# Kernel optimization log

Hardware: AMD Instinct MI355X
Metric: run time of the kernel (lower is better)

The kernel has to match this reference:

```python
import jax, jax.numpy as jnp
import numpy as np

N_NODES = 100000
N_EDGES = 1600000
IN_CH = 128
OUT_CH = 64

def setup_inputs() -> dict:
    key = jax.random.key(0)
    k = jax.random.split(key, 7)
    x = jax.random.normal(k[0], (N_NODES, IN_CH), dtype=jnp.float32)
    edge_index = jax.random.randint(k[1], (2, N_EDGES), 0, N_NODES, dtype=jnp.int64)
    neg_edge_index = jax.random.randint(k[2], (2, N_EDGES), 0, N_NODES, dtype=jnp.int64)
    # GCNConv weight [in, out] + bias, Linear classifier [2*out, 2] + bias
    W = jax.random.normal(k[3], (IN_CH, OUT_CH), dtype=jnp.float32) / np.sqrt(IN_CH)
    b = jnp.zeros((OUT_CH,), dtype=jnp.float32)
    Wc = jax.random.normal(k[4], (2 * OUT_CH, 2), dtype=jnp.float32) / np.sqrt(2 * OUT_CH)
    bc = jnp.zeros((2,), dtype=jnp.float32)
    return {"x": x, "edge_index": edge_index, "neg_edge_index": neg_edge_index,
            "W": W, "b": b, "Wc": Wc, "bc": bc}

def reference(x, edge_index, neg_edge_index, W, b, Wc, bc):
    N = x.shape[0]
    # --- GCNConv: linear transform, add self-loops, symmetric deg normalization ---
    h = x @ W                                   # [N, out]
    loops = jnp.arange(N, dtype=edge_index.dtype)
    row = jnp.concatenate([edge_index[0], loops])   # source
    col = jnp.concatenate([edge_index[1], loops])   # target
    deg = jax.ops.segment_sum(jnp.ones(col.shape, h.dtype), col, num_segments=N)
    dinv = jnp.where(deg > 0, jax.lax.rsqrt(deg), 0.0)
    norm = dinv[row] * dinv[col]                # [E+N]
    agg = jax.ops.segment_sum(h[row] * norm[:, None], col, num_segments=N)
    z = jax.nn.relu(agg + b)                    # [N, out]
    # --- edge feature gather (pos + neg edges) + linear classifier ---
    total = jnp.concatenate([edge_index, neg_edge_index], axis=1)  # [2, 2E]
    feats = jnp.concatenate([z[total[0]], z[total[1]]], axis=1)    # [2E, 2*out]
    return feats @ Wc + bc                      # [2E, 2]
```

## Files before the change

### kernel.cpp

```cpp
#include <hip/hip_runtime.h>

#define IN_CH 128
#define OUT_CH 64
#define MAXBKT 256
#define CAPB   9216
#define CHUNK  3328

typedef __attribute__((ext_vector_type(8))) short short8v;
typedef __attribute__((ext_vector_type(4))) float float4v;

union Pack { short8v s8; unsigned u[4]; };

__device__ __forceinline__ unsigned short f2bf(float f) {
    unsigned u = __float_as_uint(f);
    return (unsigned short)((u + 0x7fffu + ((u >> 16) & 1u)) >> 16);
}
__device__ __forceinline__ unsigned pk2(float a, float b) {
    return ((unsigned)f2bf(b) << 16) | (unsigned)f2bf(a);
}
__device__ __forceinline__ float bflo(unsigned d) { return __uint_as_float(d << 16); }
__device__ __forceinline__ float bfhi(unsigned d) { return __uint_as_float(d & 0xffff0000u); }

__global__ void k_zero_cnt(unsigned* __restrict__ cnt, int n) {
    int i = blockIdx.x * blockDim.x + threadIdx.x;
    if (i < n) cnt[i] = 0u;
}

__global__ __launch_bounds__(256) void k_binA(const int* __restrict__ ei,
                                              unsigned* __restrict__ bucketCount,
                                              unsigned* __restrict__ binned,
                                              int E, int nbkt) {
    __shared__ unsigned hist[MAXBKT];
    __shared__ unsigned resv[MAXBKT];
    __shared__ int colS[CHUNK];
    int tid = threadIdx.x;
    int start = blockIdx.x * CHUNK;
    int end = start + CHUNK; if (end > E) end = E;
    int cnt = end - start;

    for (int i = tid; i < MAXBKT; i += 256) hist[i] = 0u;
    __syncthreads();

    for (int i = tid; i < cnt; i += 256) {
        int c = ei[E + start + i];
        colS[i] = c;
        atomicAdd(&hist[c >> 9], 1u);
    }
    __syncthreads();

    if (tid < nbkt) {
        resv[tid] = atomicAdd(&bucketCount[tid], hist[tid]);
        hist[tid] = 0u;
    }
    __syncthreads();

    for (int i = tid; i < cnt; i += 256) {
        int c = colS[i];
        int r = ei[start + i];
        int bkt = c >> 9;
        unsigned rank = atomicAdd(&hist[bkt], 1u);
        unsigned idx = resv[bkt] + rank;
        if (idx < CAPB)
            binned[(size_t)bkt * CAPB + idx] = ((unsigned)r << 9) | (unsigned)(c & 511);
    }
}

__global__ __launch_bounds__(1024) void k_csrB(const unsigned* __restrict__ binned,
                                               const unsigned* __restrict__ bucketCount,
                                               int* __restrict__ rows,
                                               unsigned* __restrict__ offs,
                                               unsigned* __restrict__ deg,
                                               float* __restrict__ dinv, int N, int nbkt) {
    __shared__ unsigned bcnt[MAXBKT];
    __shared__ unsigned bscan[MAXBKT];
    __shared__ unsigned hist[512];
    __shared__ unsigned excl[512];
    __shared__ unsigned stage[CAPB];
    int tid = threadIdx.x;
    int b = blockIdx.x;

    if (tid < MAXBKT) {
        unsigned v = (tid < nbkt) ? bucketCount[tid] : 0u;
        if (v > (unsigned)CAPB) v = (unsigned)CAPB;
        bcnt[tid] = v;
        bscan[tid] = v;
    }
    __syncthreads();
    for (int d = 1; d < MAXBKT; d <<= 1) {
        unsigned x = 0u;
        if (tid < MAXBKT) x = bscan[tid] + ((tid >= d) ? bscan[tid - d] : 0u);
        __syncthreads();
        if (tid < MAXBKT) bscan[tid] = x;
        __syncthreads();
    }
    unsigned cnt   = bcnt[b];
    unsigned gbase = bscan[b] - cnt;
    int nodeBase = b << 9;
    int nn = N - nodeBase; if (nn > 512) nn = 512;

    for (int i = tid; i < 512; i += 1024) hist[i] = 0u;
    __syncthreads();

    const unsigned* src = binned + (size_t)b * CAPB;
    for (unsigned i = tid; i < cnt; i += 1024) {
        unsigned p = src[i];
        stage[i] = p;
        atomicAdd(&hist[p & 511u], 1u);
    }
    __syncthreads();

    if (tid < 512) excl[tid] = hist[tid];
    __syncthreads();
    for (int d = 1; d < 512; d <<= 1) {
        unsigned x = 0u;
        if (tid < 512) x = excl[tid] + ((tid >= d) ? excl[tid - d] : 0u);
        __syncthreads();
        if (tid < 512) excl[tid] = x;
        __syncthreads();
    }
    if (tid < 512) excl[tid] -= hist[tid];
    __syncthreads();

    if (tid < nn) {
        unsigned d = hist[tid];
        offs[nodeBase + tid] = gbase + excl[tid];
        deg[nodeBase + tid]  = d;
        dinv[nodeBase + tid] = rsqrtf((float)d + 1.0f);
    }
    __syncthreads();
    for (int i = tid; i < 512; i += 1024) hist[i] = 0u;
    __syncthreads();

    for (unsigned i = tid; i < cnt; i += 1024) {
        unsigned p = stage[i];
        unsigned c = p & 511u;
        unsigned r = atomicAdd(&hist[c], 1u);
        rows[gbase + excl[c] + r] = (int)(p >> 9);
    }
}

__global__ __launch_bounds__(256) void k_gemm_h(const float* __restrict__ x,
                                                const float* __restrict__ W,
                                                const float* __restrict__ dinv,
                                                unsigned short* __restrict__ hs,
                                                int N, int nChunks) {
    __shared__ float Wl[IN_CH * 66];
    int tid = threadIdx.x;
    int wid = tid >> 6;
    int l   = tid & 63;
    int g   = l >> 4;
    int m   = l & 15;

    const float4* W4 = (const float4*)W;
#pragma unroll
    for (int j = 0; j < 8; ++j) {
        int i4 = tid + j * 256;
        float4 w = W4[i4];
        int i = i4 * 4;
        int k = i >> 6, c = i & 63;
        float* dst = Wl + k * 66 + c;
        dst[0] = w.x; dst[1] = w.y; dst[2] = w.z; dst[3] = w.w;
    }
    __syncthreads();

    short8v bf[4][4];
#pragma unroll
    for (int s = 0; s < 4; ++s)
#pragma unroll
        for (int t = 0; t < 4; ++t) {
            Pack p;
#pragma unroll
            for (int jj = 0; jj < 4; ++jj) {
                int k = s * 32 + g * 8 + 2 * jj;
                float f0 = Wl[(k + 0) * 66 + t * 16 + m];
                float f1 = Wl[(k + 1) * 66 + t * 16 + m];
                p.u[jj] = pk2(f0, f1);
            }
            bf[s][t] = p.s8;
        }

    const float4* x4 = (const float4*)x;
    for (int chunk = blockIdx.x; chunk < nChunks; chunk += gridDim.x) {
        int R0 = chunk * 64 + wid * 16;
        int rowA = R0 + m; if (rowA > N - 1) rowA = N - 1;
        float4v acc[4];
#pragma unroll
        for (int t = 0; t < 4; ++t) acc[t] = (float4v){0.f, 0.f, 0.f, 0.f};

#pragma unroll
        for (int s = 0; s < 4; ++s) {
            const float4* ap = x4 + (size_t)rowA * 32 + s * 8 + g * 2;
            float4 a0 = ap[0];
            float4 a1 = ap[1];
            Pack pa;
            pa.u[0] = pk2(a0.x, a0.y);
            pa.u[1] = pk2(a0.z, a0.w);
            pa.u[2] = pk2(a1.x, a1.y);
            pa.u[3] = pk2(a1.z, a1.w);
#pragma unroll
            for (int t = 0; t < 4; ++t)
                acc[t] = __builtin_amdgcn_mfma_f32_16x16x32_bf16(pa.s8, bf[s][t], acc[t], 0, 0, 0);
        }

        int rbase = R0 + g * 4;
        float4 dv = *(const float4*)(dinv + rbase);
#pragma unroll
        for (int r = 0; r < 4; ++r) {
            int row = rbase + r;
            if (row < N) {
                float dvr = (r == 0) ? dv.x : (r == 1) ? dv.y : (r == 2) ? dv.z : dv.w;
#pragma unroll
                for (int t = 0; t < 4; ++t)
                    hs[(size_t)row * OUT_CH + t * 16 + m] = f2bf(acc[t][r] * dvr);
            }
        }
    }
}

__global__ __launch_bounds__(256) void k_gather(const unsigned* __restrict__ offs,
                                                const unsigned* __restrict__ deg,
                                                const int* __restrict__ rows,
                                                const unsigned* __restrict__ hsd,
                                                const float* __restrict__ dinv,
                                                const float* __restrict__ b,
                                                const float* __restrict__ Wc,
                                                float* __restrict__ u,
                                                float* __restrict__ v, int n) {
    int lane = threadIdx.x & 63;
    int half = lane >> 5;
    int l32  = lane & 31;
    int node = blockIdx.x * (blockDim.x >> 6) + (threadIdx.x >> 6);
    if (node >= n) return;
    unsigned start = offs[node];
    unsigned cnt = deg[node];
    const int* rp = rows + start;

    unsigned ds = hsd[((size_t)node << 5) + l32];
    float acc0 = half ? 0.f : bflo(ds);
    float acc1 = half ? 0.f : bfhi(ds);

#define GATHER_ROUND(R)                                                   \
    {                                                                     \
        int rr[R]; unsigned dd[R]; int vv[R];                             \
        _Pragma("unroll") for (int s = 0; s < R; ++s) {                   \
            int e = (int)t0 + 2 * s + half;                               \
            vv[s] = (e <= npm1);                                          \
            rr[s] = __shfl(myidx, vv[s] ? e : npm1);                      \
        }                                                                 \
        _Pragma("unroll") for (int s = 0; s < R; ++s)                     \
            dd[s] = hsd[((size_t)rr[s] << 5) + l32];                      \
        _Pragma("unroll") for (int s = 0; s < R; ++s) {                   \
            unsigned d = vv[s] ? dd[s] : 0u;                              \
            acc0 += bflo(d);                                              \
            acc1 += bfhi(d);                                              \
        }                                                                 \
        t0 += 2 * R;                                                      \
    }

    for (unsigned j0 = 0; j0 < cnt; j0 += 64) {
        unsigned rem = cnt - j0;
        unsigned np = rem < 64u ? rem : 64u;
        int npm1 = (int)np - 1;
        int myidx = rp[j0 + (lane < (int)np ? lane : 0)];

        unsigned t0 = 0;
        GATHER_ROUND(8)
        while (t0 < np) GATHER_ROUND(4)
    }
#undef GATHER_ROUND

    acc0 += __shfl_xor(acc0, 32);
    acc1 += __shfl_xor(acc1, 32);

    float di = dinv[node];
    float2 bv = ((const float2*)b)[l32];
    float z0 = fmaxf(fmaf(acc0, di, bv.x), 0.f);
    float z1 = fmaxf(fmaf(acc1, di, bv.y), 0.f);

    float4 wa = ((const float4*)Wc)[l32];
    float4 wb = ((const float4*)(Wc + 128))[l32];
    float u0 = z0 * wa.x + z1 * wa.z;
    float u1 = z0 * wa.y + z1 * wa.w;
    float v0 = z0 * wb.x + z1 * wb.z;
    float v1 = z0 * wb.y + z1 * wb.w;
#pragma unroll
    for (int off = 16; off > 0; off >>= 1) {
        u0 += __shfl_down(u0, off);
        u1 += __shfl_down(u1, off);
        v0 += __shfl_down(v0, off);
        v1 += __shfl_down(v1, off);
    }
    if (lane == 0) {
        u[node * 2 + 0] = u0;
        u[node * 2 + 1] = u1;
        v[node * 2 + 0] = v0;
        v[node * 2 + 1] = v1;
    }
}

__global__ void k_edges(const int* __restrict__ ei, const int* __restrict__ nei,
                        const float* __restrict__ u, const float* __restrict__ v,
                        const float* __restrict__ bc, float* __restrict__ out, int E) {
    int i = blockIdx.x * blockDim.x + threadIdx.x;
    int quads = E >> 1;
    if (i >= quads) return;
    int halfQ = quads >> 1;
    const int* base = (i < halfQ) ? ei : nei;
    int pi = (i < halfQ) ? i : i - halfQ;
    int4 ss = ((const int4*)base)[pi];
    int4 dd = ((const int4*)(base + E))[pi];
    float2 u0 = ((const float2*)u)[ss.x];
    float2 u1 = ((const float2*)u)[ss.y];
    float2 u2 = ((const float2*)u)[ss.z];
    float2 u3 = ((const float2*)u)[ss.w];
    float2 v0 = ((const float2*)v)[dd.x];
    float2 v1 = ((const float2*)v)[dd.y];
    float2 v2 = ((const float2*)v)[dd.z];
    float2 v3 = ((const float2*)v)[dd.w];
    float b0 = bc[0], b1 = bc[1];
    float4 r0, r1;
    r0.x = u0.x + v0.x + b0;  r0.y = u0.y + v0.y + b1;
    r0.z = u1.x + v1.x + b0;  r0.w = u1.y + v1.y + b1;
    r1.x = u2.x + v2.x + b0;  r1.y = u2.y + v2.y + b1;
    r1.z = u3.x + v3.x + b0;  r1.w = u3.y + v3.y + b1;
    ((float4*)out)[2 * i + 0] = r0;
    ((float4*)out)[2 * i + 1] = r1;
}

extern "C" void kernel_launch(void* const* d_in, const int* in_sizes, int n_in,
                              void* d_out, int out_size, void* d_ws, size_t ws_size,
                              hipStream_t stream) {
    const float* x   = (const float*)d_in[0];
    const int*   ei  = (const int*)d_in[1];
    const int*   nei = (const int*)d_in[2];
    const float* W   = (const float*)d_in[3];
    const float* b   = (const float*)d_in[4];
    const float* Wc  = (const float*)d_in[5];
    const float* bc  = (const float*)d_in[6];
    float* out = (float*)d_out;

    const int N = in_sizes[0] / IN_CH;
    const int E = in_sizes[1] / 2;
    const int nbkt = (N + 511) >> 9;
    const int nChunks = (N + 63) / 64;

    char* ws = (char*)d_ws;
    size_t off = 0;
    unsigned short* hs = (unsigned short*)(ws + off); off += (size_t)N * OUT_CH * 2;
    unsigned* binned = (unsigned*)(ws + off); off += (size_t)MAXBKT * CAPB * 4;
    int*      rows   = (int*)(ws + off);      off += (size_t)E * 4;
    unsigned* offs   = (unsigned*)(ws + off); off += (size_t)N * 4;
    unsigned* deg    = (unsigned*)(ws + off); off += (size_t)N * 4;
    float*    dinv   = (float*)(ws + off);    off += (size_t)N * 4;
    float*    u      = (float*)(ws + off);    off += (size_t)N * 2 * 4;
    float*    v      = (float*)(ws + off);    off += (size_t)N * 2 * 4;
    unsigned* bucketCount = (unsigned*)(ws + off); off += (size_t)MAXBKT * 4;

    k_zero_cnt<<<1, 256, 0, stream>>>(bucketCount, MAXBKT);
    k_binA<<<(E + CHUNK - 1) / CHUNK, 256, 0, stream>>>(ei, bucketCount, binned, E, nbkt);
    k_csrB<<<nbkt, 1024, 0, stream>>>(binned, bucketCount, rows, offs, deg, dinv, N, nbkt);
    k_gemm_h<<<512, 256, 0, stream>>>(x, W, dinv, hs, N, nChunks);
    k_gather<<<(N + 3) / 4, 256, 0, stream>>>(offs, deg, rows, (const unsigned*)hs, dinv, b, Wc, u, v, N);
    k_edges<<<(E / 2 + 255) / 256, 256, 0, stream>>>(ei, nei, u, v, bc, out, E);
}
```

Measured before the change: 140.5 us.

## Pad CSR neighbor lists to multiples of 16 with a zero sentinel row

Each node's neighbor list is padded to a multiple of 16 entries that point to a zeroed sentinel row N in hs. This removes the validity masking and tail rounds from the gather loop. Buckets now get fixed per-bucket offsets in rows, which drops the cross-bucket prefix scan in k_csrB. The classifier projection is also split across the two half-waves with xor reductions. In exchange the rows buffer is larger and the padding adds extra gathers of the sentinel row, averaging about 7.5 per node at mean degree 16.

```diff
diff --git a/kernel.cpp b/kernel.cpp
--- a/kernel.cpp
+++ b/kernel.cpp
@@ -4,6 +4,7 @@
 #define OUT_CH 64
 #define MAXBKT 256
 #define CAPB   9216
+#define CAPB_PAD 18432
 #define CHUNK  3328
 
 typedef __attribute__((ext_vector_type(8))) short short8v;
@@ -69,32 +70,17 @@
                                                const unsigned* __restrict__ bucketCount,
                                                int* __restrict__ rows,
                                                unsigned* __restrict__ offs,
-                                               unsigned* __restrict__ deg,
+                                               unsigned* __restrict__ degPad,
                                                float* __restrict__ dinv, int N, int nbkt) {
-    __shared__ unsigned bcnt[MAXBKT];
-    __shared__ unsigned bscan[MAXBKT];
     __shared__ unsigned hist[512];
+    __shared__ unsigned dpad[512];
     __shared__ unsigned excl[512];
     __shared__ unsigned stage[CAPB];
     int tid = threadIdx.x;
     int b = blockIdx.x;
-
-    if (tid < MAXBKT) {
-        unsigned v = (tid < nbkt) ? bucketCount[tid] : 0u;
-        if (v > (unsigned)CAPB) v = (unsigned)CAPB;
-        bcnt[tid] = v;
-        bscan[tid] = v;
-    }
-    __syncthreads();
-    for (int d = 1; d < MAXBKT; d <<= 1) {
-        unsigned x = 0u;
-        if (tid < MAXBKT) x = bscan[tid] + ((tid >= d) ? bscan[tid - d] : 0u);
-        __syncthreads();
-        if (tid < MAXBKT) bscan[tid] = x;
-        __syncthreads();
-    }
-    unsigned cnt   = bcnt[b];
-    unsigned gbase = bscan[b] - cnt;
+    unsigned cnt = bucketCount[b];
+    if (cnt > (unsigned)CAPB) cnt = (unsigned)CAPB;
+    size_t gbase = (size_t)b * CAPB_PAD;
     int nodeBase = b << 9;
     int nn = N - nodeBase; if (nn > 512) nn = 512;
 
@@ -109,7 +95,12 @@
     }
     __syncthreads();
 
-    if (tid < 512) excl[tid] = hist[tid];
+    if (tid < 512) {
+        unsigned d = hist[tid];
+        unsigned dp = (d + 15u) & ~15u;
+        dpad[tid] = dp;
+        excl[tid] = dp;
+    }
     __syncthreads();
     for (int d = 1; d < 512; d <<= 1) {
         unsigned x = 0u;
@@ -118,14 +109,14 @@
         if (tid < 512) excl[tid] = x;
         __syncthreads();
     }
-    if (tid < 512) excl[tid] -= hist[tid];
+    if (tid < 512) excl[tid] -= dpad[tid];
     __syncthreads();
 
     if (tid < nn) {
         unsigned d = hist[tid];
-        offs[nodeBase + tid] = gbase + excl[tid];
-        deg[nodeBase + tid]  = d;
-        dinv[nodeBase + tid] = rsqrtf((float)d + 1.0f);
+        offs[nodeBase + tid]   = (unsigned)gbase + excl[tid];
+        degPad[nodeBase + tid] = dpad[tid];
+        dinv[nodeBase + tid]   = rsqrtf((float)d + 1.0f);
     }
     __syncthreads();
     for (int i = tid; i < 512; i += 1024) hist[i] = 0u;
@@ -136,6 +127,12 @@
         unsigned c = p & 511u;
         unsigned r = atomicAdd(&hist[c], 1u);
         rows[gbase + excl[c] + r] = (int)(p >> 9);
+    }
+    __syncthreads();
+    if (tid < nn) {
+        unsigned d = hist[tid], dp = dpad[tid];
+        size_t base = gbase + excl[tid];
+        for (unsigned p = d; p < dp; ++p) rows[base + p] = N;
     }
 }
 
@@ -151,6 +148,9 @@
     int g   = l >> 4;
     int m   = l & 15;
 
+    if (blockIdx.x == 0 && tid < 32)
+        ((unsigned*)hs)[((size_t)N << 5) + tid] = 0u;
+
     const float4* W4 = (const float4*)W;
 #pragma unroll
     for (int j = 0; j < 8; ++j) {
@@ -218,7 +218,7 @@
 }
 
 __global__ __launch_bounds__(256) void k_gather(const unsigned* __restrict__ offs,
-                                                const unsigned* __restrict__ deg,
+                                                const unsigned* __restrict__ degPad,
                                                 const int* __restrict__ rows,
                                                 const unsigned* __restrict__ hsd,
                                                 const float* __restrict__ dinv,
@@ -232,42 +232,34 @@
     int node = blockIdx.x * (blockDim.x >> 6) + (threadIdx.x >> 6);
     if (node >= n) return;
     unsigned start = offs[node];
-    unsigned cnt = deg[node];
+    unsigned cntP = degPad[node];
     const int* rp = rows + start;
 
     unsigned ds = hsd[((size_t)node << 5) + l32];
     float acc0 = half ? 0.f : bflo(ds);
     float acc1 = half ? 0.f : bfhi(ds);
 
-#define GATHER_ROUND(R)                                                   \
-    {                                                                     \
-        int rr[R]; unsigned dd[R]; int vv[R];                             \
-        _Pragma("unroll") for (int s = 0; s < R; ++s) {                   \
-            int e = (int)t0 + 2 * s + half;                               \
-            vv[s] = (e <= npm1);                                          \
-            rr[s] = __shfl(myidx, vv[s] ? e : npm1);                      \
-        }                                                                 \
-        _Pragma("unroll") for (int s = 0; s < R; ++s)                     \
-            dd[s] = hsd[((size_t)rr[s] << 5) + l32];                      \
-        _Pragma("unroll") for (int s = 0; s < R; ++s) {                   \
-            unsigned d = vv[s] ? dd[s] : 0u;                              \
-            acc0 += bflo(d);                                              \
-            acc1 += bfhi(d);                                              \
-        }                                                                 \
-        t0 += 2 * R;                                                      \
-    }
-
-    for (unsigned j0 = 0; j0 < cnt; j0 += 64) {
-        unsigned rem = cnt - j0;
+    for (unsigned j0 = 0; j0 < cntP; j0 += 64) {
+        unsigned rem = cntP - j0;
         unsigned np = rem < 64u ? rem : 64u;
-        int npm1 = (int)np - 1;
         int myidx = rp[j0 + (lane < (int)np ? lane : 0)];
 
-        unsigned t0 = 0;
-        GATHER_ROUND(8)
-        while (t0 < np) GATHER_ROUND(4)
-    }
-#undef GATHER_ROUND
+        for (unsigned t0 = 0; t0 < np; t0 += 16) {
+            int rr[8];
+#pragma unroll
+            for (int s = 0; s < 8; ++s)
+                rr[s] = __shfl(myidx, (int)t0 + 2 * s + half);
+            unsigned dd[8];
+#pragma unroll
+            for (int s = 0; s < 8; ++s)
+                dd[s] = hsd[((size_t)rr[s] << 5) + l32];
+#pragma unroll
+            for (int s = 0; s < 8; ++s) {
+                acc0 += bflo(dd[s]);
+                acc1 += bfhi(dd[s]);
+            }
+        }
+    }
 
     acc0 += __shfl_xor(acc0, 32);
     acc1 += __shfl_xor(acc1, 32);
@@ -277,25 +269,17 @@
     float z0 = fmaxf(fmaf(acc0, di, bv.x), 0.f);
     float z1 = fmaxf(fmaf(acc1, di, bv.y), 0.f);
 
-    float4 wa = ((const float4*)Wc)[l32];
-    float4 wb = ((const float4*)(Wc + 128))[l32];
-    float u0 = z0 * wa.x + z1 * wa.z;
-    float u1 = z0 * wa.y + z1 * wa.w;
-    float v0 = z0 * wb.x + z1 * wb.z;
-    float v1 = z0 * wb.y + z1 * wb.w;
+    float4 w = ((const float4*)(Wc + (half ? 128 : 0)))[l32];
+    float p0 = z0 * w.x + z1 * w.z;
+    float p1 = z0 * w.y + z1 * w.w;
 #pragma unroll
     for (int off = 16; off > 0; off >>= 1) {
-        u0 += __shfl_down(u0, off);
-        u1 += __shfl_down(u1, off);
-        v0 += __shfl_down(v0, off);
-        v1 += __shfl_down(v1, off);
-    }
-    if (lane == 0) {
-        u[node * 2 + 0] = u0;
-        u[node * 2 + 1] = u1;
-        v[node * 2 + 0] = v0;
-        v[node * 2 + 1] = v1;
-    }
+        p0 += __shfl_xor(p0, off);
+        p1 += __shfl_xor(p1, off);
+    }
+    float2 r; r.x = p0; r.y = p1;
+    if (lane == 0)  ((float2*)u)[node] = r;
+    if (lane == 32) ((float2*)v)[node] = r;
 }
 
 __global__ void k_edges(const int* __restrict__ ei, const int* __restrict__ nei,
@@ -346,11 +330,11 @@
 
     char* ws = (char*)d_ws;
     size_t off = 0;
-    unsigned short* hs = (unsigned short*)(ws + off); off += (size_t)N * OUT_CH * 2;
+    unsigned short* hs = (unsigned short*)(ws + off); off += ((size_t)N + 1) * OUT_CH * 2;
     unsigned* binned = (unsigned*)(ws + off); off += (size_t)MAXBKT * CAPB * 4;
-    int*      rows   = (int*)(ws + off);      off += (size_t)E * 4;
+    int*      rows   = (int*)(ws + off);      off += (size_t)MAXBKT * CAPB_PAD * 4;
     unsigned* offs   = (unsigned*)(ws + off); off += (size_t)N * 4;
-    unsigned* deg    = (unsigned*)(ws + off); off += (size_t)N * 4;
+    unsigned* degP   = (unsigned*)(ws + off); off += (size_t)N * 4;
     float*    dinv   = (float*)(ws + off);    off += (size_t)N * 4;
     float*    u      = (float*)(ws + off);    off += (size_t)N * 2 * 4;
     float*    v      = (float*)(ws + off);    off += (size_t)N * 2 * 4;
@@ -358,8 +342,8 @@
 
     k_zero_cnt<<<1, 256, 0, stream>>>(bucketCount, MAXBKT);
     k_binA<<<(E + CHUNK - 1) / CHUNK, 256, 0, stream>>>(ei, bucketCount, binned, E, nbkt);
-    k_csrB<<<nbkt, 1024, 0, stream>>>(binned, bucketCount, rows, offs, deg, dinv, N, nbkt);
+    k_csrB<<<nbkt, 1024, 0, stream>>>(binned, bucketCount, rows, offs, degP, dinv, N, nbkt);
     k_gemm_h<<<512, 256, 0, stream>>>(x, W, dinv, hs, N, nChunks);
-    k_gather<<<(N + 3) / 4, 256, 0, stream>>>(offs, deg, rows, (const unsigned*)hs, dinv, b, Wc, u, v, N);
+    k_gather<<<(N + 3) / 4, 256, 0, stream>>>(offs, degP, rows, (const unsigned*)hs, dinv, b, Wc, u, v, N);
     k_edges<<<(E / 2 + 255) / 256, 256, 0, stream>>>(ei, nei, u, v, bc, out, E);
 }
```

Result: no change. 138.3 us (-1.6%).
